# Kernel optimization log

Hardware: AMD Instinct MI355X
Metric: run time of the kernel (lower is better)

Reference implementation:

```python
import jax, jax.numpy as jnp
import numpy as np

NEG = -1e30  # finite stand-in for -inf so softmax grads stay clean


def setup_inputs() -> dict:
    key = jax.random.key(0)
    k1, k2 = jax.random.split(key)
    C, D = 8192, 512
    gt_class_embeddings = jax.random.normal(k1, (C, D), dtype=jnp.float32)
    w = jax.random.normal(k2, (C, D), dtype=jnp.float32)
    return {"gt_class_embeddings": gt_class_embeddings, "w": w}


def reference(gt_class_embeddings, w):
    # L2-normalize class embeddings, cosine-similarity matrix S (diag == 1)
    G = gt_class_embeddings / jnp.linalg.norm(gt_class_embeddings, axis=-1, keepdims=True)
    S = G @ G.T  # [C, C]
    C = S.shape[0]
    off_diag = ~jnp.eye(C, dtype=bool)

    # seSoftmax: per-row softmax over entries != 1 (off-diagonal); diagonal stays 1
    P = jax.nn.softmax(jnp.where(off_diag, S, NEG), axis=-1)
    S2 = jnp.where(off_diag, P, 1.0)

    # argsort(-S2)[1] == most similar (diag value 1 always ranks first),
    # argsort(-S2)[-1] == least similar == row min (softmax values < 1)
    ms = jnp.argmax(jnp.where(off_diag, S2, NEG), axis=-1)  # [C]
    ls = jnp.argmin(jnp.where(off_diag, S2, -NEG), axis=-1)  # [C]

    rows = jnp.arange(C)
    margin = S2[rows, ms] - S2[rows, ls]  # [C]

    d_ms = jnp.sqrt(jnp.sum((w - w[ms]) ** 2, axis=-1))  # [C]
    d_ls = jnp.sqrt(jnp.sum((w - w[ls]) ** 2, axis=-1))  # [C]

    loss = jnp.mean(jnp.maximum(0.0, d_ms - d_ls + margin))
    return loss
```

## Files before the change

kernel.cpp:

```cpp
#include <hip/hip_runtime.h>
#include <math.h>

#define CDIM 8192
#define DDIM 512
#define NEGF -3.0e38f
#define POSF  3.0e38f

#define BM 128
#define NSLOT (CDIM / BM)

typedef __attribute__((ext_vector_type(8))) short bf16x8;
typedef __attribute__((ext_vector_type(4))) float f32x4;

__device__ __forceinline__ unsigned short f2bf(float x) {
    unsigned int u = __float_as_uint(x);
    u += 0x7fffu + ((u >> 16) & 1u);
    return (unsigned short)(u >> 16);
}
__device__ __forceinline__ float bf2f(unsigned short h) {
    return __uint_as_float(((unsigned int)h) << 16);
}
__device__ __forceinline__ void gld16(const void* g, void* l) {
    __builtin_amdgcn_global_load_lds(
        (__attribute__((address_space(1))) void*)(void*)g,
        (__attribute__((address_space(3))) void*)l, 16, 0, 0);
}

__global__ __launch_bounds__(256) void k_prep(const float* __restrict__ g,
                                              unsigned short* __restrict__ hi,
                                              unsigned short* __restrict__ lo) {
    const int wave = threadIdx.x >> 6;
    const int lane = threadIdx.x & 63;
    const int row = blockIdx.x * 4 + wave;
    const float4* src = (const float4*)(g + (size_t)row * DDIM);
    const float4 a = src[lane * 2];
    const float4 b = src[lane * 2 + 1];
    float s = a.x * a.x + a.y * a.y + a.z * a.z + a.w * a.w +
              b.x * b.x + b.y * b.y + b.z * b.z + b.w * b.w;
#pragma unroll
    for (int m = 1; m < 64; m <<= 1) s += __shfl_xor(s, m, 64);
    const float rn = rsqrtf(s);
    const float y[8] = {a.x * rn, a.y * rn, a.z * rn, a.w * rn,
                        b.x * rn, b.y * rn, b.z * rn, b.w * rn};
    unsigned int hv[4], lv[4];
#pragma unroll
    for (int i = 0; i < 4; ++i) {
        const unsigned short h0 = f2bf(y[2 * i]);
        const unsigned short h1 = f2bf(y[2 * i + 1]);
        const unsigned short l0 = f2bf(y[2 * i] - bf2f(h0));
        const unsigned short l1 = f2bf(y[2 * i + 1] - bf2f(h1));
        hv[i] = (unsigned int)h0 | ((unsigned int)h1 << 16);
        lv[i] = (unsigned int)l0 | ((unsigned int)l1 << 16);
    }
    uint4* dh = (uint4*)(hi + (size_t)row * DDIM + lane * 8);
    uint4* dl = (uint4*)(lo + (size_t)row * DDIM + lane * 8);
    *dh = make_uint4(hv[0], hv[1], hv[2], hv[3]);
    *dl = make_uint4(lv[0], lv[1], lv[2], lv[3]);
}

__device__ __constant__ unsigned char OSUP[28] = {
    1, 2, 10,   3, 11, 19,   4, 12, 20,   28, 5, 13,
    21, 29, 37, 6,   14, 22, 30, 38,   46, 7, 15, 23,   31, 39, 47, 55};

__global__ __launch_bounds__(256, 3) void k_simstats(
    const unsigned short* __restrict__ ghi, const unsigned short* __restrict__ glo,
    float* __restrict__ pmax, float* __restrict__ pmin, float* __restrict__ pZ,
    int* __restrict__ pamax, int* __restrict__ pamin) {
    const int bid = blockIdx.x;
    const int xcd = bid & 7;
    const int off = bid >> 3;
    int I, J;
    if (xcd < 4) {
        if (off < 72) {
            const int s = xcd * 2 + (off >= 36);
            const int u = (off >= 36) ? off - 36 : off;
            int jj = 0;
            while ((jj + 1) * (jj + 2) / 2 <= u) ++jj;
            const int ii = u - jj * (jj + 1) / 2;
            I = s * 8 + ii; J = s * 8 + jj;
        } else {
            const int sup = (off - 72) >> 6;
            const int u = (off - 72) & 63;
            const int code = OSUP[xcd * 3 + sup];
            I = (code >> 3) * 8 + (u & 7);
            J = (code & 7) * 8 + (u >> 3);
        }
    } else {
        if (off >= 256) return;
        const int sup = off >> 6;
        const int u = off & 63;
        const int code = OSUP[12 + (xcd - 4) * 4 + sup];
        I = (code >> 3) * 8 + (u & 7);
        J = (code & 7) * 8 + (u >> 3);
    }

    __shared__ unsigned short SH[4 * BM * 32];
    unsigned short* Ahi = SH;
    unsigned short* Alo = SH + 4096;
    unsigned short* Bhi = SH + 8192;
    unsigned short* Blo = SH + 12288;
    const int t = threadIdx.x;
    const int wave = t >> 6;
    const int lane = t & 63;
    const int lanelo = lane & 15;
    const int quad = lane >> 4;
    const int wr = wave & 1;
    const int wc = wave >> 1;

    const int srow = t >> 2;
    const int scolb = ((t & 3) ^ ((t >> 3) & 3)) << 4;
    char* lAh = (char*)Ahi + t * 16;
    char* lAl = (char*)Alo + t * 16;
    char* lBh = (char*)Bhi + t * 16;
    char* lBl = (char*)Blo + t * 16;

    const int fsl = (quad ^ ((lanelo >> 1) & 3)) << 3;
    const int aoff = (wr * 64 + lanelo) * 32 + fsl;
    const int boff = (wc * 64 + lanelo) * 32 + fsl;

    float* rm  = (float*)SH;
    float* rz  = rm + 256;
    float* rmn = rz + 256;
    int*   ra  = (int*)(rmn + 256);
    int*   ran = ra + 256;
    float* cm  = (float*)Bhi;
    float* cz  = cm + 256;
    float* cmn = cz + 256;
    int*   ca  = (int*)(cmn + 256);
    int*   can = ca + 256;

    const int i0 = I * BM;
    const int j0 = J * BM;
    const bool isdiag = (I == J);

    f32x4 acc[4][4];
#pragma unroll
    for (int rt = 0; rt < 4; ++rt)
#pragma unroll
        for (int ct = 0; ct < 4; ++ct)
            acc[rt][ct] = (f32x4){0.f, 0.f, 0.f, 0.f};

    const char* baseAh = (const char*)ghi + (size_t)(i0 + srow) * 1024 + scolb;
    const char* baseAl = (const char*)glo + (size_t)(i0 + srow) * 1024 + scolb;
    const char* baseBh = (const char*)ghi + (size_t)(j0 + srow) * 1024 + scolb;
    const char* baseBl = (const char*)glo + (size_t)(j0 + srow) * 1024 + scolb;

    for (int k0 = 0; k0 < DDIM; k0 += 32) {
        __syncthreads();
#pragma unroll
        for (int q = 0; q < 2; ++q) {
            const size_t roff = (size_t)q * 64 * 1024 + k0 * 2;
            gld16(baseAh + roff, lAh + q * 4096);
            gld16(baseAl + roff, lAl + q * 4096);
            gld16(baseBh + roff, lBh + q * 4096);
            gld16(baseBl + roff, lBl + q * 4096);
        }
        __syncthreads();
        bf16x8 ah[4], al[4];
#pragma unroll
        for (int rt = 0; rt < 4; ++rt) {
            ah[rt] = *(const bf16x8*)&Ahi[aoff + rt * 512];
            al[rt] = *(const bf16x8*)&Alo[aoff + rt * 512];
        }
#pragma unroll
        for (int ct = 0; ct < 4; ++ct) {
            const bf16x8 bh = *(const bf16x8*)&Bhi[boff + ct * 512];
            const bf16x8 bl = *(const bf16x8*)&Blo[boff + ct * 512];
#pragma unroll
            for (int rt = 0; rt < 4; ++rt) {
                acc[rt][ct] = __builtin_amdgcn_mfma_f32_16x16x32_bf16(
                    ah[rt], bh, acc[rt][ct], 0, 0, 0);
                acc[rt][ct] = __builtin_amdgcn_mfma_f32_16x16x32_bf16(
                    ah[rt], bl, acc[rt][ct], 0, 0, 0);
                acc[rt][ct] = __builtin_amdgcn_mfma_f32_16x16x32_bf16(
                    al[rt], bh, acc[rt][ct], 0, 0, 0);
            }
        }
    }

    __syncthreads();

#pragma unroll
    for (int rt = 0; rt < 4; ++rt) {
#pragma unroll
        for (int r = 0; r < 4; ++r) {
            const int lrow = wr * 64 + rt * 16 + quad * 4 + r;
            float tmax = NEGF; int targ = 0;
            float tmin = POSF; int targn = 0;
            if (isdiag) {
                const int gi = i0 + lrow;
#pragma unroll
                for (int ct = 0; ct < 4; ++ct) {
                    const int gj = j0 + wc * 64 + ct * 16 + lanelo;
                    const float v = acc[rt][ct][r];
                    const bool dg = (gj == gi);
                    const float vM = dg ? NEGF : v;
                    const float vm = dg ? POSF : v;
                    if (vM > tmax) { tmax = vM; targ = gj; }
                    if (vm < tmin) { tmin = vm; targn = gj; }
                }
            } else {
#pragma unroll
                for (int ct = 0; ct < 4; ++ct) {
                    const int gj = j0 + wc * 64 + ct * 16 + lanelo;
                    const float v = acc[rt][ct][r];
                    if (v > tmax) { tmax = v; targ = gj; }
                    if (v < tmin) { tmin = v; targn = gj; }
                }
            }
#pragma unroll
            for (int msk = 1; msk < 16; msk <<= 1) {
                const float v2 = __shfl_xor(tmax, msk, 64);
                const int i2 = __shfl_xor(targ, msk, 64);
                if (v2 > tmax) { tmax = v2; targ = i2; }
                const float v3 = __shfl_xor(tmin, msk, 64);
                const int i3 = __shfl_xor(targn, msk, 64);
                if (v3 < tmin) { tmin = v3; targn = i3; }
            }
            if (lanelo == 0) {
                const int o = wc * 128 + lrow;
                rm[o] = tmax; rmn[o] = tmin;
                ra[o] = targ; ran[o] = targn;
            }
        }
    }

    if (!isdiag) {
#pragma unroll
        for (int ct = 0; ct < 4; ++ct) {
            const int lcol = wc * 64 + ct * 16 + lanelo;
            float tmax = NEGF; int targ = 0;
            float tmin = POSF; int targn = 0;
#pragma unroll
            for (int rt = 0; rt < 4; ++rt)
#pragma unroll
                for (int r = 0; r < 4; ++r) {
                    const int gi = i0 + wr * 64 + rt * 16 + quad * 4 + r;
                    const float v = acc[rt][ct][r];
                    if (v > tmax) { tmax = v; targ = gi; }
                    if (v < tmin) { tmin = v; targn = gi; }
                }
#pragma unroll
            for (int msk = 16; msk < 64; msk <<= 1) {
                const float m2 = __shfl_xor(tmax, msk, 64);
                const int i2 = __shfl_xor(targ, msk, 64);
                if (m2 > tmax) { tmax = m2; targ = i2; }
                const float mn2 = __shfl_xor(tmin, msk, 64);
                const int in2 = __shfl_xor(targn, msk, 64);
                if (mn2 < tmin) { tmin = mn2; targn = in2; }
            }
            if (quad == 0) {
                const int o = wr * 128 + lcol;
                cm[o] = tmax; cmn[o] = tmin;
                ca[o] = targ; can[o] = targn;
            }
        }
    }

#pragma unroll
    for (int rt = 0; rt < 4; ++rt)
#pragma unroll
        for (int ct = 0; ct < 4; ++ct)
#pragma unroll
            for (int r = 0; r < 4; ++r)
                acc[rt][ct][r] = __expf(acc[rt][ct][r] - 1.f);
    if (isdiag && wr == wc) {
#pragma unroll
        for (int rt = 0; rt < 4; ++rt)
#pragma unroll
            for (int r = 0; r < 4; ++r)
                if (lanelo == quad * 4 + r) acc[rt][rt][r] = 0.f;
    }

#pragma unroll
    for (int rt = 0; rt < 4; ++rt)
#pragma unroll
        for (int r = 0; r < 4; ++r) {
            float s = acc[rt][0][r] + acc[rt][1][r] +
                      acc[rt][2][r] + acc[rt][3][r];
#pragma unroll
            for (int msk = 1; msk < 16; msk <<= 1) s += __shfl_xor(s, msk, 64);
            if (lanelo == 0)
                rz[wc * 128 + wr * 64 + rt * 16 + quad * 4 + r] = s;
        }

    if (!isdiag) {
#pragma unroll
        for (int ct = 0; ct < 4; ++ct) {
            float s = 0.f;
#pragma unroll
            for (int rt = 0; rt < 4; ++rt)
                s += acc[rt][ct][0] + acc[rt][ct][1] +
                     acc[rt][ct][2] + acc[rt][ct][3];
#pragma unroll
            for (int msk = 16; msk < 64; msk <<= 1) s += __shfl_xor(s, msk, 64);
            if (quad == 0)
                cz[wr * 128 + wc * 64 + ct * 16 + lanelo] = s;
        }
    }

    __syncthreads();

    if (t < BM) {
        const float m0 = rm[t], m1 = rm[128 + t];
        float vmax = m0; int imax = ra[t];
        if (m1 > vmax) { vmax = m1; imax = ra[128 + t]; }
        float vmin = rmn[t]; int imin = ran[t];
        if (rmn[128 + t] < vmin) { vmin = rmn[128 + t]; imin = ran[128 + t]; }
        const size_t o = (size_t)J * CDIM + i0 + t;
        pmax[o] = vmax; pmin[o] = vmin; pZ[o] = rz[t] + rz[128 + t];
        pamax[o] = imax; pamin[o] = imin;
    } else if (!isdiag) {
        const int tt = t - BM;
        const float m0 = cm[tt], m1 = cm[128 + tt];
        float vmax = m0; int imax = ca[tt];
        if (m1 > vmax) { vmax = m1; imax = ca[128 + tt]; }
        float vmin = cmn[tt]; int imin = can[tt];
        if (cmn[128 + tt] < vmin) { vmin = cmn[128 + tt]; imin = can[128 + tt]; }
        const size_t o = (size_t)I * CDIM + j0 + tt;
        pmax[o] = vmax; pmin[o] = vmin; pZ[o] = cz[tt] + cz[128 + tt];
        pamax[o] = imax; pamin[o] = imin;
    }
}

__global__ __launch_bounds__(256) void k_lossc(
    const float* __restrict__ pmax, const float* __restrict__ pmin,
    const float* __restrict__ pZ, const int* __restrict__ pamax,
    const int* __restrict__ pamin, const float* __restrict__ w,
    float* __restrict__ vals) {
    const int wave = threadIdx.x >> 6;
    const int lane = threadIdx.x & 63;
    const int row = blockIdx.x * 4 + wave;
    const size_t o = (size_t)lane * CDIM + row;
    float v = pmax[o]; int a = pamax[o];
    float u = pmin[o]; int b = pamin[o];
    float z = pZ[o];
#pragma unroll
    for (int msk = 1; msk < 64; msk <<= 1) {
        const float v2 = __shfl_xor(v, msk, 64);
        const int i2 = __shfl_xor(a, msk, 64);
        if (v2 > v) { v = v2; a = i2; }
        const float v3 = __shfl_xor(u, msk, 64);
        const int i3 = __shfl_xor(b, msk, 64);
        if (v3 < u) { u = v3; b = i3; }
        z += __shfl_xor(z, msk, 64);
    }
    const float margin = (1.f - __expf(u - v)) * __expf(v - 1.f) / z;
    const int jm = a, jl = b;

    const float4* wi = (const float4*)(w + (size_t)row * DDIM);
    const float4* wm = (const float4*)(w + (size_t)jm * DDIM);
    const float4* wl = (const float4*)(w + (size_t)jl * DDIM);
    float sm = 0.f, sl = 0.f;
#pragma unroll
    for (int h = 0; h < 2; ++h) {
        const int idx = h * 64 + lane;
        const float4 x = wi[idx];
        const float4 y = wm[idx];
        const float4 c = wl[idx];
        float d;
        d = x.x - y.x; sm = fmaf(d, d, sm);
        d = x.y - y.y; sm = fmaf(d, d, sm);
        d = x.z - y.z; sm = fmaf(d, d, sm);
        d = x.w - y.w; sm = fmaf(d, d, sm);
        d = x.x - c.x; sl = fmaf(d, d, sl);
        d = x.y - c.y; sl = fmaf(d, d, sl);
        d = x.z - c.z; sl = fmaf(d, d, sl);
        d = x.w - c.w; sl = fmaf(d, d, sl);
    }
#pragma unroll
    for (int msk = 1; msk < 64; msk <<= 1) {
        sm += __shfl_xor(sm, msk, 64);
        sl += __shfl_xor(sl, msk, 64);
    }
    if (lane == 0) {
        const float val = sqrtf(sm) - sqrtf(sl) + margin;
        vals[row] = val > 0.f ? val : 0.f;
    }
}

__global__ __launch_bounds__(256) void k_final(const float* __restrict__ vals,
                                               float* __restrict__ out) {
    __shared__ float red[256];
    float s = 0.f;
    for (int i = threadIdx.x; i < CDIM; i += 256) s += vals[i];
    red[threadIdx.x] = s;
    __syncthreads();
#pragma unroll
    for (int k = 128; k > 0; k >>= 1) {
        if (threadIdx.x < (unsigned)k) red[threadIdx.x] += red[threadIdx.x + k];
        __syncthreads();
    }
    if (threadIdx.x == 0) out[0] = red[0] * (1.0f / CDIM);
}

extern "C" void kernel_launch(void* const* d_in, const int* in_sizes, int n_in,
                              void* d_out, int out_size, void* d_ws, size_t ws_size,
                              hipStream_t stream) {
    const float* g = (const float*)d_in[0];
    const float* w = (const float*)d_in[1];
    float* out = (float*)d_out;

    unsigned short* ghi = (unsigned short*)d_ws;
    unsigned short* glo = ghi + (size_t)CDIM * DDIM;
    float* p = (float*)(glo + (size_t)CDIM * DDIM);
    float* pmax = p;      p += (size_t)NSLOT * CDIM;
    float* pmin = p;      p += (size_t)NSLOT * CDIM;
    float* pZ = p;        p += (size_t)NSLOT * CDIM;
    int* pamax = (int*)p; p += (size_t)NSLOT * CDIM;
    int* pamin = (int*)p; p += (size_t)NSLOT * CDIM;
    float* vals = p;      p += CDIM;

    k_prep<<<CDIM / 4, 256, 0, stream>>>(g, ghi, glo);
    k_simstats<<<2112, 256, 0, stream>>>(ghi, glo, pmax, pmin, pZ, pamax, pamin);
    k_lossc<<<CDIM / 4, 256, 0, stream>>>(pmax, pmin, pZ, pamax, pamin, w, vals);
    k_final<<<1, 256, 0, stream>>>(vals, out);
}
```

Baseline: 230.9 us.

## Fuse loss and final reduction into simstats via per-band completion counters

New measurement: 415.9 us. +80.1%, slower.

```diff
diff --git a/kernel.cpp b/kernel.cpp
--- a/kernel.cpp
+++ b/kernel.cpp
@@ -26,50 +26,11 @@
         (__attribute__((address_space(3))) void*)l, 16, 0, 0);
 }
 
-__global__ __launch_bounds__(256) void k_prep(const float* __restrict__ g,
-                                              unsigned short* __restrict__ hi,
-                                              unsigned short* __restrict__ lo) {
-    const int wave = threadIdx.x >> 6;
-    const int lane = threadIdx.x & 63;
-    const int row = blockIdx.x * 4 + wave;
-    const float4* src = (const float4*)(g + (size_t)row * DDIM);
-    const float4 a = src[lane * 2];
-    const float4 b = src[lane * 2 + 1];
-    float s = a.x * a.x + a.y * a.y + a.z * a.z + a.w * a.w +
-              b.x * b.x + b.y * b.y + b.z * b.z + b.w * b.w;
-#pragma unroll
-    for (int m = 1; m < 64; m <<= 1) s += __shfl_xor(s, m, 64);
-    const float rn = rsqrtf(s);
-    const float y[8] = {a.x * rn, a.y * rn, a.z * rn, a.w * rn,
-                        b.x * rn, b.y * rn, b.z * rn, b.w * rn};
-    unsigned int hv[4], lv[4];
-#pragma unroll
-    for (int i = 0; i < 4; ++i) {
-        const unsigned short h0 = f2bf(y[2 * i]);
-        const unsigned short h1 = f2bf(y[2 * i + 1]);
-        const unsigned short l0 = f2bf(y[2 * i] - bf2f(h0));
-        const unsigned short l1 = f2bf(y[2 * i + 1] - bf2f(h1));
-        hv[i] = (unsigned int)h0 | ((unsigned int)h1 << 16);
-        lv[i] = (unsigned int)l0 | ((unsigned int)l1 << 16);
-    }
-    uint4* dh = (uint4*)(hi + (size_t)row * DDIM + lane * 8);
-    uint4* dl = (uint4*)(lo + (size_t)row * DDIM + lane * 8);
-    *dh = make_uint4(hv[0], hv[1], hv[2], hv[3]);
-    *dl = make_uint4(lv[0], lv[1], lv[2], lv[3]);
-}
-
 __device__ __constant__ unsigned char OSUP[28] = {
     1, 2, 10,   3, 11, 19,   4, 12, 20,   28, 5, 13,
     21, 29, 37, 6,   14, 22, 30, 38,   46, 7, 15, 23,   31, 39, 47, 55};
 
-__global__ __launch_bounds__(256, 3) void k_simstats(
-    const unsigned short* __restrict__ ghi, const unsigned short* __restrict__ glo,
-    float* __restrict__ pmax, float* __restrict__ pmin, float* __restrict__ pZ,
-    int* __restrict__ pamax, int* __restrict__ pamin) {
-    const int bid = blockIdx.x;
-    const int xcd = bid & 7;
-    const int off = bid >> 3;
-    int I, J;
+__device__ __forceinline__ void tile_map(int xcd, int off, int& I, int& J) {
     if (xcd < 4) {
         if (off < 72) {
             const int s = xcd * 2 + (off >= 36);
@@ -86,20 +47,54 @@
             J = (code & 7) * 8 + (u >> 3);
         }
     } else {
-        if (off >= 256) return;
         const int sup = off >> 6;
         const int u = off & 63;
         const int code = OSUP[12 + (xcd - 4) * 4 + sup];
         I = (code >> 3) * 8 + (u & 7);
         J = (code & 7) * 8 + (u >> 3);
     }
-
-    __shared__ unsigned short SH[4 * BM * 32];
+}
+
+
+__device__ __forceinline__ void prep_row(const float* __restrict__ g,
+                                         unsigned short* __restrict__ hi,
+                                         unsigned short* __restrict__ lo,
+                                         int row, int lane) {
+    const float4* src = (const float4*)(g + (size_t)row * DDIM);
+    const float4 a = src[lane * 2];
+    const float4 b = src[lane * 2 + 1];
+    float s = a.x * a.x + a.y * a.y + a.z * a.z + a.w * a.w +
+              b.x * b.x + b.y * b.y + b.z * b.z + b.w * b.w;
+#pragma unroll
+    for (int m = 1; m < 64; m <<= 1) s += __shfl_xor(s, m, 64);
+    const float rn = rsqrtf(s);
+    const float y[8] = {a.x * rn, a.y * rn, a.z * rn, a.w * rn,
+                        b.x * rn, b.y * rn, b.z * rn, b.w * rn};
+    unsigned int hv[4], lv[4];
+#pragma unroll
+    for (int i = 0; i < 4; ++i) {
+        const unsigned short h0 = f2bf(y[2 * i]);
+        const unsigned short h1 = f2bf(y[2 * i + 1]);
+        const unsigned short l0 = f2bf(y[2 * i] - bf2f(h0));
+        const unsigned short l1 = f2bf(y[2 * i + 1] - bf2f(h1));
+        hv[i] = (unsigned int)h0 | ((unsigned int)h1 << 16);
+        lv[i] = (unsigned int)l0 | ((unsigned int)l1 << 16);
+    }
+    uint4* dh = (uint4*)(hi + (size_t)row * DDIM + lane * 8);
+    uint4* dl = (uint4*)(lo + (size_t)row * DDIM + lane * 8);
+    *dh = make_uint4(hv[0], hv[1], hv[2], hv[3]);
+    *dl = make_uint4(lv[0], lv[1], lv[2], lv[3]);
+}
+
+__device__ __forceinline__ void simstats_tile(
+    const unsigned short* __restrict__ ghi, const unsigned short* __restrict__ glo,
+    float* __restrict__ pmax, float* __restrict__ pmin, float* __restrict__ pZ,
+    int* __restrict__ pamax, int* __restrict__ pamin,
+    unsigned short* SH, int I, int J, int t) {
     unsigned short* Ahi = SH;
     unsigned short* Alo = SH + 4096;
     unsigned short* Bhi = SH + 8192;
     unsigned short* Blo = SH + 12288;
-    const int t = threadIdx.x;
     const int wave = t >> 6;
     const int lane = t & 63;
     const int lanelo = lane & 15;
@@ -323,14 +318,11 @@
     }
 }
 
-__global__ __launch_bounds__(256) void k_lossc(
+__device__ __forceinline__ void lossc_row(
     const float* __restrict__ pmax, const float* __restrict__ pmin,
     const float* __restrict__ pZ, const int* __restrict__ pamax,
     const int* __restrict__ pamin, const float* __restrict__ w,
-    float* __restrict__ vals) {
-    const int wave = threadIdx.x >> 6;
-    const int lane = threadIdx.x & 63;
-    const int row = blockIdx.x * 4 + wave;
+    float* __restrict__ vals, int row, int lane) {
     const size_t o = (size_t)lane * CDIM + row;
     float v = pmax[o]; int a = pamax[o];
     float u = pmin[o]; int b = pamin[o];
@@ -379,19 +371,85 @@
     }
 }
 
-__global__ __launch_bounds__(256) void k_final(const float* __restrict__ vals,
-                                               float* __restrict__ out) {
-    __shared__ float red[256];
+__device__ __forceinline__ void final_mean(const float* __restrict__ vals,
+                                           float* __restrict__ out,
+                                           float* red, int t) {
     float s = 0.f;
-    for (int i = threadIdx.x; i < CDIM; i += 256) s += vals[i];
-    red[threadIdx.x] = s;
+    for (int i = t; i < CDIM; i += 256) s += vals[i];
+    red[t] = s;
     __syncthreads();
 #pragma unroll
     for (int k = 128; k > 0; k >>= 1) {
-        if (threadIdx.x < (unsigned)k) red[threadIdx.x] += red[threadIdx.x + k];
+        if (t < k) red[t] += red[t + k];
         __syncthreads();
     }
-    if (threadIdx.x == 0) out[0] = red[0] * (1.0f / CDIM);
+    if (t == 0) out[0] = red[0] * (1.0f / CDIM);
+}
+
+__global__ __launch_bounds__(256) void k_prep(const float* __restrict__ g,
+                                              unsigned short* __restrict__ hi,
+                                              unsigned short* __restrict__ lo,
+                                              int* __restrict__ ctrz) {
+    if (blockIdx.x == 0 && threadIdx.x < 65) ctrz[threadIdx.x] = 0;
+    const int wave = threadIdx.x >> 6;
+    const int lane = threadIdx.x & 63;
+    prep_row(g, hi, lo, blockIdx.x * 4 + wave, lane);
+}
+
+__global__ __launch_bounds__(256, 3) void k_simstats(
+    const unsigned short* __restrict__ ghi, const unsigned short* __restrict__ glo,
+    float* __restrict__ pmax, float* __restrict__ pmin, float* __restrict__ pZ,
+    int* __restrict__ pamax, int* __restrict__ pamin,
+    const float* __restrict__ w, float* __restrict__ vals,
+    int* __restrict__ bandc, int* __restrict__ done2, float* __restrict__ out) {
+    __shared__ unsigned short SH[4 * BM * 32];
+    __shared__ int s_ownR, s_ownC, s_fin;
+    const int bid = blockIdx.x;
+    const int xcd = bid & 7;
+    const int off = bid >> 3;
+    if (xcd >= 4 && off >= 256) return;
+    int I, J;
+    tile_map(xcd, off, I, J);
+    const int t = threadIdx.x;
+    const int wave = t >> 6;
+    const int lane = t & 63;
+
+    simstats_tile(ghi, glo, pmax, pmin, pZ, pamax, pamin, SH, I, J, t);
+
+    __syncthreads();
+    if (t == 0) {
+        __threadfence();
+        s_ownR = (atomicAdd(&bandc[I], 1) + 1 == 64);
+        s_ownC = (I != J) && (atomicAdd(&bandc[J], 1) + 1 == 64);
+    }
+    __syncthreads();
+
+    const int nown = (s_ownR ? 1 : 0) + (s_ownC ? 1 : 0);
+    if (nown) {
+        __threadfence();
+        if (s_ownR) {
+#pragma unroll 2
+            for (int rr = wave; rr < BM; rr += 4)
+                lossc_row(pmax, pmin, pZ, pamax, pamin, w, vals,
+                          I * BM + rr, lane);
+        }
+        if (s_ownC) {
+#pragma unroll 2
+            for (int rr = wave; rr < BM; rr += 4)
+                lossc_row(pmax, pmin, pZ, pamax, pamin, w, vals,
+                          J * BM + rr, lane);
+        }
+        __syncthreads();
+        if (t == 0) {
+            __threadfence();
+            s_fin = (atomicAdd(done2, nown) + nown == 64);
+        }
+        __syncthreads();
+        if (s_fin) {
+            __threadfence();
+            final_mean(vals, out, (float*)SH, t);
+        }
+    }
 }
 
 extern "C" void kernel_launch(void* const* d_in, const int* in_sizes, int n_in,
@@ -410,9 +468,10 @@
     int* pamax = (int*)p; p += (size_t)NSLOT * CDIM;
     int* pamin = (int*)p; p += (size_t)NSLOT * CDIM;
     float* vals = p;      p += CDIM;
-
-    k_prep<<<CDIM / 4, 256, 0, stream>>>(g, ghi, glo);
-    k_simstats<<<2112, 256, 0, stream>>>(ghi, glo, pmax, pmin, pZ, pamax, pamin);
-    k_lossc<<<CDIM / 4, 256, 0, stream>>>(pmax, pmin, pZ, pamax, pamin, w, vals);
-    k_final<<<1, 256, 0, stream>>>(vals, out);
-}
+    int* bandc = (int*)p;
+    int* done2 = bandc + 64;
+
+    k_prep<<<CDIM / 4, 256, 0, stream>>>(g, ghi, glo, bandc);
+    k_simstats<<<2112, 256, 0, stream>>>(ghi, glo, pmax, pmin, pZ, pamax,
+                                         pamin, w, vals, bandc, done2, out);
+}
```
